# Optimization experiments

Hardware: AMD Instinct MI355X
Metric: run time of the kernel (lower is better)

## Reference

```python
import jax, jax.numpy as jnp
import numpy as np

DT = 1.0  # module init dt

def setup_inputs() -> dict:
    key = jax.random.key(0)
    k1, k2 = jax.random.split(key)
    x = jax.random.normal(k1, (8, 4096, 512), dtype=jnp.float32)
    w = jax.random.normal(k2, (512,), dtype=jnp.float32)
    return {"x": x, "w": w}

def reference(x, w):
    # h_t = h_{t-1} + dt*(x_t - relu(w)*h_{t-1}) = a*h_{t-1} + dt*x_t,  a = 1 - dt*relu(w)
    a = (1.0 - DT * jax.nn.relu(w)).astype(x.dtype)  # [d]
    h0 = jnp.zeros((x.shape[0], x.shape[2]), dtype=x.dtype)  # [b, d]
    xt = jnp.swapaxes(x, 0, 1)  # [t, b, d]

    def step(h, x_t):
        h_next = a * h + DT * x_t
        return h_next, h_next

    _, hs = jax.lax.scan(step, h0, xt)  # [t, b, d]
    return jnp.swapaxes(hs, 0, 1)  # [b, t, d] (return_sequences=True)
```

## Files before the change

### kernel.cpp

```cpp
#include <hip/hip_runtime.h>


#define RB 8
#define RT 4096
#define RD 512
#define RC 64
#define RL 64
#define DG (RD / 4)

#define HB 1e15f

__device__ __forceinline__ float sclamp(float v) {
    return fminf(fmaxf(v, -HB), HB);
}

__global__ void __launch_bounds__(DG)
k_carry(const float4* __restrict__ x4, const float4* __restrict__ w4,
        float4* __restrict__ Lc) {
    const int g  = threadIdx.x;
    const int bc = blockIdx.x;
    const int b  = bc >> 6;
    const int c  = bc & (RC - 1);

    const float4 wv = w4[g];
    const float ax = 1.0f - fmaxf(wv.x, 0.0f);
    const float ay = 1.0f - fmaxf(wv.y, 0.0f);
    const float az = 1.0f - fmaxf(wv.z, 0.0f);
    const float aw = 1.0f - fmaxf(wv.w, 0.0f);

    const float4* __restrict__ xp = x4 + ((size_t)b * RT + (size_t)c * RL) * DG + g;

    float hx = 0.f, hy = 0.f, hz = 0.f, hw = 0.f;
#pragma unroll 8
    for (int i = 0; i < RL; ++i) {
        const float4 v = xp[(size_t)i * DG];
        hx = sclamp(ax * hx + v.x);
        hy = sclamp(ay * hy + v.y);
        hz = sclamp(az * hz + v.z);
        hw = sclamp(aw * hw + v.w);
    }
    Lc[(size_t)bc * DG + g] = make_float4(hx, hy, hz, hw);
}

__global__ void __launch_bounds__(DG)
k_final(const float4* __restrict__ x4, const float4* __restrict__ w4,
        const float4* __restrict__ Lc, float4* __restrict__ out4) {
    const int g  = threadIdx.x;
    const int bc = blockIdx.x;
    const int b  = bc >> 6;
    const int c  = bc & (RC - 1);

    const float4 wv = w4[g];
    const float ax = 1.0f - fmaxf(wv.x, 0.0f);
    const float ay = 1.0f - fmaxf(wv.y, 0.0f);
    const float az = 1.0f - fmaxf(wv.z, 0.0f);
    const float aw = 1.0f - fmaxf(wv.w, 0.0f);

    float Ax = ax, Ay = ay, Az = az, Aw = aw;
#pragma unroll
    for (int i = 0; i < 6; ++i) {
        Ax = sclamp(Ax * Ax); Ay = sclamp(Ay * Ay);
        Az = sclamp(Az * Az); Aw = sclamp(Aw * Aw);
    }

    const float4* __restrict__ lp = Lc + (size_t)b * RC * DG + g;
    float hx = 0.f, hy = 0.f, hz = 0.f, hw = 0.f;
    for (int j = 0; j < c; ++j) {
        const float4 L = lp[(size_t)j * DG];
        hx = sclamp(Ax * hx + L.x);
        hy = sclamp(Ay * hy + L.y);
        hz = sclamp(Az * hz + L.z);
        hw = sclamp(Aw * hw + L.w);
    }

    const float4* __restrict__ xp = x4   + ((size_t)b * RT + (size_t)c * RL) * DG + g;
    float4*       __restrict__ op = out4 + ((size_t)b * RT + (size_t)c * RL) * DG + g;
#pragma unroll 8
    for (int i = 0; i < RL; ++i) {
        const float4 v = xp[(size_t)i * DG];
        hx = sclamp(ax * hx + v.x);
        hy = sclamp(ay * hy + v.y);
        hz = sclamp(az * hz + v.z);
        hw = sclamp(aw * hw + v.w);
        op[(size_t)i * DG] = make_float4(hx, hy, hz, hw);
    }
}

__global__ void __launch_bounds__(256)
rnn_seq_sat(const float* __restrict__ x, const float* __restrict__ w,
            float* __restrict__ out) {
    const int idx = blockIdx.x * blockDim.x + threadIdx.x;
    if (idx >= RB * RD) return;
    const int b = idx >> 9;
    const int d = idx & (RD - 1);
    const float a = 1.0f - fmaxf(w[d], 0.0f);
    const float* xp = x + (size_t)b * RT * RD + d;
    float* op = out + (size_t)b * RT * RD + d;
    float h = 0.f;
#pragma unroll 4
    for (int t = 0; t < RT; ++t) {
        h = sclamp(a * h + xp[(size_t)t * RD]);
        op[(size_t)t * RD] = h;
    }
}

extern "C" void kernel_launch(void* const* d_in, const int* in_sizes, int n_in,
                              void* d_out, int out_size, void* d_ws, size_t ws_size,
                              hipStream_t stream) {
    const float* x = (const float*)d_in[0];
    const float* w = (const float*)d_in[1];
    float* out = (float*)d_out;

    const size_t need = (size_t)RB * RC * DG * sizeof(float4);
    if (ws_size >= need) {
        const float4* x4 = (const float4*)x;
        const float4* w4 = (const float4*)w;
        float4* Lc = (float4*)d_ws;
        k_carry<<<dim3(RB * RC), dim3(DG), 0, stream>>>(x4, w4, Lc);
        k_final<<<dim3(RB * RC), dim3(DG), 0, stream>>>(x4, w4, Lc, (float4*)out);
    } else {
        rnn_seq_sat<<<dim3((RB * RD) / 256), dim3(256), 0, stream>>>(x, w, out);
    }
}
```

Before: 127.0 us.

## Fuse carry and final passes into one kernel with per-batch atomic barrier

Merges the chunk-carry kernel and the final scan kernel into a single launch. Each block publishes its chunk carry, bumps a per-batch atomic counter, and blocks with c>0 spin until all 64 chunks of their batch are done, then combine carries and rescan their chunk. This removes one kernel launch and the gap between launches, and keeps the chunk's x data warm in cache for the second pass. It adds a memset of the counters and depends on all 512 blocks being co-resident, since a spin-wait on blocks that never get scheduled would deadlock.

```diff
diff --git a/kernel.cpp b/kernel.cpp
--- a/kernel.cpp
+++ b/kernel.cpp
@@ -15,8 +15,9 @@
 }
 
 __global__ void __launch_bounds__(DG)
-k_carry(const float4* __restrict__ x4, const float4* __restrict__ w4,
-        float4* __restrict__ Lc) {
+rnn_fused(const float4* __restrict__ x4, const float4* __restrict__ w4,
+          float4* __restrict__ out4, float4* __restrict__ Lc,
+          unsigned int* __restrict__ cnt) {
     const int g  = threadIdx.x;
     const int bc = blockIdx.x;
     const int b  = bc >> 6;
@@ -40,41 +41,42 @@
         hw = sclamp(aw * hw + v.w);
     }
     Lc[(size_t)bc * DG + g] = make_float4(hx, hy, hz, hw);
-}
 
-__global__ void __launch_bounds__(DG)
-k_final(const float4* __restrict__ x4, const float4* __restrict__ w4,
-        const float4* __restrict__ Lc, float4* __restrict__ out4) {
-    const int g  = threadIdx.x;
-    const int bc = blockIdx.x;
-    const int b  = bc >> 6;
-    const int c  = bc & (RC - 1);
-
-    const float4 wv = w4[g];
-    const float ax = 1.0f - fmaxf(wv.x, 0.0f);
-    const float ay = 1.0f - fmaxf(wv.y, 0.0f);
-    const float az = 1.0f - fmaxf(wv.z, 0.0f);
-    const float aw = 1.0f - fmaxf(wv.w, 0.0f);
-
-    float Ax = ax, Ay = ay, Az = az, Aw = aw;
-#pragma unroll
-    for (int i = 0; i < 6; ++i) {
-        Ax = sclamp(Ax * Ax); Ay = sclamp(Ay * Ay);
-        Az = sclamp(Az * Az); Aw = sclamp(Aw * Aw);
+    __syncthreads();
+    if (g == 0) {
+        __hip_atomic_fetch_add(&cnt[b], 1u, __ATOMIC_RELEASE,
+                               __HIP_MEMORY_SCOPE_AGENT);
     }
 
-    const float4* __restrict__ lp = Lc + (size_t)b * RC * DG + g;
-    float hx = 0.f, hy = 0.f, hz = 0.f, hw = 0.f;
-    for (int j = 0; j < c; ++j) {
-        const float4 L = lp[(size_t)j * DG];
-        hx = sclamp(Ax * hx + L.x);
-        hy = sclamp(Ay * hy + L.y);
-        hz = sclamp(Az * hz + L.z);
-        hw = sclamp(Aw * hw + L.w);
+    float Hx = 0.f, Hy = 0.f, Hz = 0.f, Hw = 0.f;
+    if (c != 0) {
+        if (g == 0) {
+            while (__hip_atomic_load(&cnt[b], __ATOMIC_ACQUIRE,
+                                     __HIP_MEMORY_SCOPE_AGENT) < RC) {
+                __builtin_amdgcn_s_sleep(8);
+            }
+        }
+        __syncthreads();
+
+        float Ax = ax, Ay = ay, Az = az, Aw = aw;
+#pragma unroll
+        for (int i = 0; i < 6; ++i) {
+            Ax = sclamp(Ax * Ax); Ay = sclamp(Ay * Ay);
+            Az = sclamp(Az * Az); Aw = sclamp(Aw * Aw);
+        }
+
+        const float4* __restrict__ lp = Lc + (size_t)b * RC * DG + g;
+        for (int j = 0; j < c; ++j) {
+            const float4 L = lp[(size_t)j * DG];
+            Hx = sclamp(Ax * Hx + L.x);
+            Hy = sclamp(Ay * Hy + L.y);
+            Hz = sclamp(Az * Hz + L.z);
+            Hw = sclamp(Aw * Hw + L.w);
+        }
     }
 
-    const float4* __restrict__ xp = x4   + ((size_t)b * RT + (size_t)c * RL) * DG + g;
-    float4*       __restrict__ op = out4 + ((size_t)b * RT + (size_t)c * RL) * DG + g;
+    float4* __restrict__ op = out4 + ((size_t)b * RT + (size_t)c * RL) * DG + g;
+    hx = Hx; hy = Hy; hz = Hz; hw = Hw;
 #pragma unroll 8
     for (int i = 0; i < RL; ++i) {
         const float4 v = xp[(size_t)i * DG];
@@ -111,13 +113,14 @@
     const float* w = (const float*)d_in[1];
     float* out = (float*)d_out;
 
-    const size_t need = (size_t)RB * RC * DG * sizeof(float4);
-    if (ws_size >= need) {
-        const float4* x4 = (const float4*)x;
-        const float4* w4 = (const float4*)w;
+    const size_t lc_bytes  = (size_t)RB * RC * DG * sizeof(float4);
+    const size_t cnt_bytes = RB * sizeof(unsigned int);
+    if (ws_size >= lc_bytes + cnt_bytes) {
         float4* Lc = (float4*)d_ws;
-        k_carry<<<dim3(RB * RC), dim3(DG), 0, stream>>>(x4, w4, Lc);
-        k_final<<<dim3(RB * RC), dim3(DG), 0, stream>>>(x4, w4, Lc, (float4*)out);
+        unsigned int* cnt = (unsigned int*)((char*)d_ws + lc_bytes);
+        hipMemsetAsync(cnt, 0, cnt_bytes, stream);
+        rnn_fused<<<dim3(RB * RC), dim3(DG), 0, stream>>>(
+            (const float4*)x, (const float4*)w, (float4*)out, Lc, cnt);
     } else {
         rnn_seq_sat<<<dim3((RB * RD) / 256), dim3(256), 0, stream>>>(x, w, out);
     }
```

New measurement: 191.7 us. 1.51x slower.
